# Kernel optimization log

Hardware: AMD Instinct MI355X
Metric: run time of the kernel (lower is better)

Reference implementation:

```python
import math
import jax, jax.numpy as jnp
import numpy as np

NUM_HEADS = 8
HEAD_DIM = 64


def setup_inputs() -> dict:
    key = jax.random.key(0)
    k1, k2, k3, k4 = jax.random.split(key, 4)
    C = 256
    E = NUM_HEADS * HEAD_DIM  # 512
    x = jax.random.normal(k1, (4, C, 48, 48), dtype=jnp.float32)
    Wqkv = jax.random.normal(k2, (3 * E, C), dtype=jnp.float32) * (1.0 / math.sqrt(C))
    Wout = jax.random.normal(k3, (C, E), dtype=jnp.float32) * (1.0 / math.sqrt(E))
    bout = jax.random.normal(k4, (C,), dtype=jnp.float32) * 0.01
    return {"x": x, "Wqkv": Wqkv, "Wout": Wout, "bout": bout}


def reference(x, Wqkv, Wout, bout):
    b, c, H, W = x.shape
    nh, hd = NUM_HEADS, HEAD_DIM
    N = H * W
    scale = 1.0 / math.sqrt(hd)
    # 1x1 conv (no bias) == channel matmul
    qkv = jnp.einsum('bcxy,oc->boxy', x, Wqkv)            # [b, 3*nh*hd, H, W]
    qkv = qkv.reshape(b, 3, nh, hd, N)                    # channel split order: (k, h, d)
    q, k, v = qkv[:, 0], qkv[:, 1], qkv[:, 2]             # each [b, nh, hd, N]
    att = jnp.einsum('bhdi,bhdj->bhij', q, k) * scale     # [b, nh, N, N]
    att = jax.nn.softmax(att, axis=-1)                    # stable (max-subtract inside)
    out = jnp.einsum('bhij,bhdj->bhid', att, v)           # [b, nh, N, hd]
    out = out.transpose(0, 1, 3, 2).reshape(b, nh * hd, H, W)  # 'b h (x y) d -> b (h d) x y'
    # 1x1 conv with bias
    return jnp.einsum('bexy,ce->bcxy', out, Wout) + bout[None, :, None, None]
```

## Files before the change

### kernel.cpp

```cpp
#include <hip/hip_runtime.h>

typedef __attribute__((ext_vector_type(8))) __bf16 bf16x8;
typedef __attribute__((ext_vector_type(16))) float f32x16;
typedef __attribute__((ext_vector_type(4))) float f32x4;
typedef __attribute__((ext_vector_type(4))) unsigned short us4;

__device__ __forceinline__ unsigned short f2bf(float f) {
  __bf16 h = (__bf16)f;
  return __builtin_bit_cast(unsigned short, h);
}
__device__ __forceinline__ unsigned pack2bf(float lo, float hi) {
  return (unsigned)f2bf(lo) | ((unsigned)f2bf(hi) << 16);
}

#define GLL(src, dst)                                                            \
  __builtin_amdgcn_global_load_lds((const __attribute__((address_space(1))) void*)(src), \
                                   (__attribute__((address_space(3))) void*)(dst), 16, 0, 0)

__device__ __forceinline__ void stage_chunks(const unsigned short* g, int ld,
                                             unsigned short* lds, int rows, int tid) {
  int total = rows * 8;
  for (int c0 = 0; c0 < total; c0 += 256) {
    int c = c0 + tid;
    int row = c >> 3, kc = c & 7;
    const unsigned short* src = g + (size_t)row * ld + ((kc ^ (row & 7)) << 3);
    unsigned short* dst = lds + (size_t)(c0 + (tid & 192)) * 8;
    GLL(src, dst);
  }
}

__device__ __forceinline__ bf16x8 frag(const unsigned short* lds, int row, int kc) {
  return *(const bf16x8*)(lds + row * 64 + ((kc ^ (row & 7)) << 3));
}


__global__ void k_cvt(const float* __restrict__ in, unsigned short* __restrict__ outp, int n) {
  int i = (blockIdx.x * 256 + threadIdx.x) * 4;
  if (i + 3 < n) {
    f32x4 v = *(const f32x4*)(in + i);
    us4 o;
#pragma unroll
    for (int k = 0; k < 4; k++) o[k] = f2bf(v[k]);
    *(us4*)(outp + i) = o;
  }
}

__global__ __launch_bounds__(256) void k_xpose(const float* __restrict__ x,
                                               unsigned short* __restrict__ xT) {
  __shared__ float t[32][33];
  int tid = threadIdx.x;
  int col = tid & 31, rowb = tid >> 5;
  int nt = blockIdx.x * 32, ct = blockIdx.y * 32, b = blockIdx.z;
  const float* src = x + ((size_t)b * 256 + ct) * 2304 + nt;
#pragma unroll
  for (int rr = 0; rr < 32; rr += 8) t[rowb + rr][col] = src[(size_t)(rowb + rr) * 2304 + col];
  __syncthreads();
  unsigned short* dst = xT + ((size_t)b * 2304 + nt) * 256 + ct;
#pragma unroll
  for (int rr = 0; rr < 32; rr += 8) dst[(size_t)(rowb + rr) * 256 + col] = f2bf(t[col][rowb + rr]);
}

__global__ __launch_bounds__(256, 2) void k_gemm_qkv(
    const unsigned short* __restrict__ W, const unsigned short* __restrict__ xT,
    unsigned short* __restrict__ qT, unsigned short* __restrict__ kT,
    unsigned short* __restrict__ vv) {
  __shared__ unsigned short As[128 * 64];
  __shared__ unsigned short Bs[128 * 64];
  int tid = threadIdx.x, lane = tid & 63, wid = tid >> 6;
  int m0 = blockIdx.x * 128, n0 = blockIdx.y * 128, b = blockIdx.z;
  const unsigned short* Ag = W + (size_t)m0 * 256;
  const unsigned short* Bg = xT + ((size_t)b * 2304 + n0) * 256;
  int wm = (wid >> 1) * 64, wn = (wid & 1) * 64;
  f32x4 acc[4][4] = {};
  for (int kt = 0; kt < 256; kt += 64) {
    __syncthreads();
    stage_chunks(Ag + kt, 256, As, 128, tid);
    stage_chunks(Bg + kt, 256, Bs, 128, tid);
    __syncthreads();
#pragma unroll
    for (int kk = 0; kk < 2; kk++) {
      bf16x8 af[4], bf[4];
#pragma unroll
      for (int i = 0; i < 4; i++) af[i] = frag(As, wm + i * 16 + (lane & 15), kk * 4 + (lane >> 4));
#pragma unroll
      for (int j = 0; j < 4; j++) bf[j] = frag(Bs, wn + j * 16 + (lane & 15), kk * 4 + (lane >> 4));
#pragma unroll
      for (int i = 0; i < 4; i++)
#pragma unroll
        for (int j = 0; j < 4; j++)
          acc[i][j] = __builtin_amdgcn_mfma_f32_16x16x32_bf16(af[i], bf[j], acc[i][j], 0, 0, 0);
    }
  }
#pragma unroll
  for (int i = 0; i < 4; i++) {
    int o = m0 + wm + i * 16 + ((lane >> 4) << 2);
    int which = o >> 9, h = (o >> 6) & 7, d0 = o & 63;
#pragma unroll
    for (int j = 0; j < 4; j++) {
      int n = n0 + wn + j * 16 + (lane & 15);
      if (which == 2) {
#pragma unroll
        for (int jj = 0; jj < 4; jj++)
          vv[((size_t)(b * 8 + h) * 64 + d0 + jj) * 2304 + n] = f2bf(acc[i][j][jj]);
      } else {
        float sc = which ? 1.0f : 0.18033688011112042f;
        us4 pk;
#pragma unroll
        for (int jj = 0; jj < 4; jj++) pk[jj] = f2bf(acc[i][j][jj] * sc);
        unsigned short* dst = (which ? kT : qT) + ((size_t)(b * 8 + h) * 2304 + n) * 64 + d0;
        *(us4*)dst = pk;
      }
    }
  }
}

__global__ __launch_bounds__(512, 4) void k_attn(
    const unsigned short* __restrict__ qT, const unsigned short* __restrict__ kT,
    const unsigned short* __restrict__ vv, unsigned short* __restrict__ o2T) {
  __shared__ unsigned short L[2][4][4096];
  int tid = threadIdx.x, lane = tid & 63;
  int wid = tid >> 6, rh = wid & 3, jh = wid >> 2;
  int il = lane & 31, g = lane >> 5;
  int lin = blockIdx.x;
  int xcd = lin & 7, idx = lin >> 3;
  int bh = xcd * 4 + idx / 18;
  int i0 = (idx % 18) * 128;
  const unsigned short* kT_bh = kT + (size_t)bh * 2304 * 64;
  const unsigned short* vv_bh = vv + (size_t)bh * 64 * 2304;
  const unsigned short* qrow = qT + ((size_t)bh * 2304 + i0 + rh * 32 + il) * 64;
  bf16x8 qf[4];
#pragma unroll
  for (int ks = 0; ks < 4; ks++) qf[ks] = *(const bf16x8*)(qrow + (ks * 2 + g) * 8);

  int srow = tid >> 3, skc = tid & 7;
  unsigned sw = (unsigned)((skc ^ (srow & 7)) << 3);
  unsigned oK = srow * 64 + sw;
  unsigned oV = srow * 2304 + sw;
  int db = (tid & 448) * 8;
  unsigned short* dK0 = &L[0][0][db];
  unsigned short* dK1 = &L[0][1][db];
  unsigned short* dV0 = &L[0][2][db];
  unsigned short* dV1 = &L[0][3][db];

#define STAGE(boff)                          \
  do {                                       \
    GLL(kT_bh + oK, dK0 + (boff));           \
    GLL(kT_bh + 73728 + oK, dK1 + (boff));   \
    GLL(vv_bh + oV, dV0 + (boff));           \
    GLL(vv_bh + 1152 + oV, dV1 + (boff));    \
    oK += 4096; oV += 64;                    \
  } while (0)

  const unsigned short* fK[8];
  const unsigned short* fV[8];
#pragma unroll
  for (int ks = 0; ks < 4; ks++) {
    int cs = ks * 2 + g;
    int o0 = il * 64 + ((cs ^ (il & 7)) << 3);
    int o1 = (32 + il) * 64 + ((cs ^ (il & 7)) << 3);
    fK[ks] = &L[0][jh][o0];
    fK[4 + ks] = &L[0][jh][o1];
    fV[ks] = &L[0][2 + jh][o0];
    fV[4 + ks] = &L[0][2 + jh][o1];
  }

  float lrun = 0.f;
  f32x16 O0 = {}, O1 = {};

#define COMP(boff)                                                                        \
  do {                                                                                    \
    f32x16 S0 = {}, S1 = {};                                                              \
    __builtin_amdgcn_s_setprio(1);                                                        \
    _Pragma("unroll") for (int ks = 0; ks < 4; ks++) {                                    \
      bf16x8 kf0 = *(const bf16x8*)(fK[ks] + (boff));                                     \
      bf16x8 kf1 = *(const bf16x8*)(fK[4 + ks] + (boff));                                 \
      S0 = __builtin_amdgcn_mfma_f32_32x32x16_bf16(kf0, qf[ks], S0, 0, 0, 0);             \
      S1 = __builtin_amdgcn_mfma_f32_32x32x16_bf16(kf1, qf[ks], S1, 0, 0, 0);             \
    }                                                                                     \
    __builtin_amdgcn_s_setprio(0);                                                        \
    float a16[16];                                                                        \
    _Pragma("unroll") for (int r = 0; r < 16; r++) {                                      \
      S0[r] = __builtin_amdgcn_exp2f(S0[r]);                                              \
      S1[r] = __builtin_amdgcn_exp2f(S1[r]);                                              \
      a16[r] = S0[r] + S1[r];                                                             \
    }                                                                                     \
    _Pragma("unroll") for (int s = 8; s >= 1; s >>= 1)                                    \
        _Pragma("unroll") for (int r = 0; r < 8; r++) if (r < s) a16[r] += a16[r + s];    \
    lrun += a16[0];                                                                       \
    unsigned w0[8], w1[8];                                                                \
    _Pragma("unroll") for (int m = 0; m < 8; m++) {                                       \
      w0[m] = pack2bf(S0[2 * m], S0[2 * m + 1]);                                          \
      w1[m] = pack2bf(S1[2 * m], S1[2 * m + 1]);                                          \
    }                                                                                     \
    __builtin_amdgcn_s_setprio(1);                                                        \
    _Pragma("unroll") for (int ks = 0; ks < 4; ks++) {                                    \
      int a = ks & 1;                                                                     \
      unsigned A0, A1, B0, B1;                                                            \
      if (ks >> 1) { A0 = w1[4 * a]; A1 = w1[4 * a + 1]; B0 = w1[4 * a + 2]; B1 = w1[4 * a + 3]; } \
      else         { A0 = w0[4 * a]; A1 = w0[4 * a + 1]; B0 = w0[4 * a + 2]; B1 = w0[4 * a + 3]; } \
      unsigned send0 = g ? A0 : B0, send1 = g ? A1 : B1;                                  \
      unsigned pw0 = __shfl_xor(send0, 32), pw1 = __shfl_xor(send1, 32);                  \
      union { unsigned u[4]; bf16x8 v; } F;                                               \
      F.u[0] = g ? pw0 : A0;                                                              \
      F.u[1] = g ? pw1 : A1;                                                              \
      F.u[2] = g ? B0 : pw0;                                                              \
      F.u[3] = g ? B1 : pw1;                                                              \
      bf16x8 vf0 = *(const bf16x8*)(fV[ks] + (boff));                                     \
      bf16x8 vf1 = *(const bf16x8*)(fV[4 + ks] + (boff));                                 \
      O0 = __builtin_amdgcn_mfma_f32_32x32x16_bf16(vf0, F.v, O0, 0, 0, 0);                \
      O1 = __builtin_amdgcn_mfma_f32_32x32x16_bf16(vf1, F.v, O1, 0, 0, 0);                \
    }                                                                                     \
    __builtin_amdgcn_s_setprio(0);                                                        \
  } while (0)

  STAGE(0);
  __syncthreads();
#pragma unroll 1
  for (int it = 0; it < 9; it++) {
    STAGE(16384);
    COMP(0);
    __syncthreads();
    if (it < 8) STAGE(0);
    COMP(16384);
    __syncthreads();
  }
#undef STAGE
#undef COMP

  lrun += __shfl_xor(lrun, 32);
  float* sm = (float*)&L[0][0][0];
  float* ml = (float*)&L[1][0][0];
  if (jh == 1) {
#pragma unroll
    for (int r = 0; r < 16; r++) {
      sm[(rh * 32 + r) * 64 + lane] = O0[r];
      sm[(rh * 32 + 16 + r) * 64 + lane] = O1[r];
    }
    if (!g) ml[rh * 32 + il] = lrun;
  }
  __syncthreads();
  if (jh == 0) {
    float rl = 1.0f / (lrun + ml[rh * 32 + il]);
    int b = bh >> 3, h = bh & 7;
    unsigned short* dst = o2T + ((size_t)b * 2304 + (i0 + rh * 32 + il)) * 512 + h * 64;
#pragma unroll
    for (int dt = 0; dt < 2; dt++) {
#pragma unroll
      for (int u = 0; u < 4; u++) {
        us4 pk;
#pragma unroll
        for (int v = 0; v < 4; v++) {
          int r = 4 * u + v;
          float own = dt ? O1[r] : O0[r];
          float oth = sm[(rh * 32 + dt * 16 + r) * 64 + lane];
          pk[v] = f2bf((own + oth) * rl);
        }
        *(us4*)(dst + dt * 32 + 8 * u + 4 * g) = pk;
      }
    }
  }
}

__global__ __launch_bounds__(256, 2) void k_gemm_out(
    const unsigned short* __restrict__ Wo, const unsigned short* __restrict__ o2T,
    const float* __restrict__ bout, float* __restrict__ out) {
  __shared__ unsigned short As[128 * 64];
  __shared__ unsigned short Bs[128 * 64];
  int tid = threadIdx.x, lane = tid & 63, wid = tid >> 6;
  int m0 = blockIdx.x * 128, n0 = blockIdx.y * 128, b = blockIdx.z;
  const unsigned short* Ag = Wo + (size_t)m0 * 512;
  const unsigned short* Bg = o2T + ((size_t)b * 2304 + n0) * 512;
  int wm = (wid >> 1) * 64, wn = (wid & 1) * 64;
  f32x4 acc[4][4] = {};
  for (int kt = 0; kt < 512; kt += 64) {
    __syncthreads();
    stage_chunks(Ag + kt, 512, As, 128, tid);
    stage_chunks(Bg + kt, 512, Bs, 128, tid);
    __syncthreads();
#pragma unroll
    for (int kk = 0; kk < 2; kk++) {
      bf16x8 af[4], bf[4];
#pragma unroll
      for (int i = 0; i < 4; i++) af[i] = frag(As, wm + i * 16 + (lane & 15), kk * 4 + (lane >> 4));
#pragma unroll
      for (int j = 0; j < 4; j++) bf[j] = frag(Bs, wn + j * 16 + (lane & 15), kk * 4 + (lane >> 4));
#pragma unroll
      for (int i = 0; i < 4; i++)
#pragma unroll
        for (int j = 0; j < 4; j++)
          acc[i][j] = __builtin_amdgcn_mfma_f32_16x16x32_bf16(af[i], bf[j], acc[i][j], 0, 0, 0);
    }
  }
#pragma unroll
  for (int i = 0; i < 4; i++) {
    int c = m0 + wm + i * 16 + ((lane >> 4) << 2);
#pragma unroll
    for (int j = 0; j < 4; j++) {
      int n = n0 + wn + j * 16 + (lane & 15);
#pragma unroll
      for (int jj = 0; jj < 4; jj++)
        out[((size_t)b * 256 + c + jj) * 2304 + n] = acc[i][j][jj] + bout[c + jj];
    }
  }
}

extern "C" void kernel_launch(void* const* d_in, const int* in_sizes, int n_in,
                              void* d_out, int out_size, void* d_ws, size_t ws_size,
                              hipStream_t stream) {
  const float* x = (const float*)d_in[0];
  const float* Wqkv = (const float*)d_in[1];
  const float* Wout = (const float*)d_in[2];
  const float* bout = (const float*)d_in[3];
  float* out = (float*)d_out;
  char* ws = (char*)d_ws;
  unsigned short* Wqkv_bf = (unsigned short*)(ws + 0);
  unsigned short* Wout_bf = (unsigned short*)(ws + 786432);
  unsigned short* xT      = (unsigned short*)(ws + 1048576);
  unsigned short* qT      = (unsigned short*)(ws + 5767168);
  unsigned short* kT      = (unsigned short*)(ws + 15204352);
  unsigned short* vv      = (unsigned short*)(ws + 24641536);
  unsigned short* o2T     = (unsigned short*)(ws + 34078720);

  k_cvt<<<dim3(384), dim3(256), 0, stream>>>(Wqkv, Wqkv_bf, 1536 * 256);
  k_cvt<<<dim3(128), dim3(256), 0, stream>>>(Wout, Wout_bf, 256 * 512);
  k_xpose<<<dim3(72, 8, 4), dim3(256), 0, stream>>>(x, xT);
  k_gemm_qkv<<<dim3(12, 18, 4), dim3(256), 0, stream>>>(Wqkv_bf, xT, qT, kT, vv);
  k_attn<<<dim3(576), dim3(512), 0, stream>>>(qT, kT, vv, o2T);
  k_gemm_out<<<dim3(2, 18, 4), dim3(256), 0, stream>>>(Wout_bf, o2T, bout, out);
}
```

Before: 111.5 us.

## Merge weight conversions, defer softmax row-sum reduction, halve out-GEMM N tile

Fuses the two fp32-to-bf16 weight conversion launches into one kernel, removing a launch. In attention, per-lane partial row sums are kept in 16 registers across all key tiles and tree-reduced once at the end instead of every iteration. The row-sum scratch moves to its own shared array, and a barrier is added before shared memory is reused. The output GEMM tile shrinks from 128 to 64 columns, doubling grid size to improve occupancy on the many-CU GPU at the cost of more reloads of A.

After: 118.8 us. 6.6% more time.

```diff
diff --git a/kernel.cpp b/kernel.cpp
--- a/kernel.cpp
+++ b/kernel.cpp
@@ -34,15 +34,20 @@
 }
 
 
-__global__ void k_cvt(const float* __restrict__ in, unsigned short* __restrict__ outp, int n) {
+__global__ void k_cvt2(const float* __restrict__ wqkv, const float* __restrict__ wout,
+                       unsigned short* __restrict__ oq, unsigned short* __restrict__ oo) {
+  const int NA = 1536 * 256;
   int i = (blockIdx.x * 256 + threadIdx.x) * 4;
-  if (i + 3 < n) {
-    f32x4 v = *(const f32x4*)(in + i);
-    us4 o;
-#pragma unroll
-    for (int k = 0; k < 4; k++) o[k] = f2bf(v[k]);
-    *(us4*)(outp + i) = o;
-  }
+  const float* src;
+  unsigned short* dst;
+  int j;
+  if (i < NA) { src = wqkv; dst = oq; j = i; }
+  else        { src = wout; dst = oo; j = i - NA; }
+  f32x4 v = *(const f32x4*)(src + j);
+  us4 o;
+#pragma unroll
+  for (int k = 0; k < 4; k++) o[k] = f2bf(v[k]);
+  *(us4*)(dst + j) = o;
 }
 
 __global__ __launch_bounds__(256) void k_xpose(const float* __restrict__ x,
@@ -118,6 +123,7 @@
     const unsigned short* __restrict__ qT, const unsigned short* __restrict__ kT,
     const unsigned short* __restrict__ vv, unsigned short* __restrict__ o2T) {
   __shared__ unsigned short L[2][4][4096];
+  __shared__ float ml[128];
   int tid = threadIdx.x, lane = tid & 63;
   int wid = tid >> 6, rh = wid & 3, jh = wid >> 2;
   int il = lane & 31, g = lane >> 5;
@@ -164,7 +170,7 @@
     fV[4 + ks] = &L[0][2 + jh][o1];
   }
 
-  float lrun = 0.f;
+  float a16[16] = {};
   f32x16 O0 = {}, O1 = {};
 
 #define COMP(boff)                                                                        \
@@ -178,15 +184,11 @@
       S1 = __builtin_amdgcn_mfma_f32_32x32x16_bf16(kf1, qf[ks], S1, 0, 0, 0);             \
     }                                                                                     \
     __builtin_amdgcn_s_setprio(0);                                                        \
-    float a16[16];                                                                        \
     _Pragma("unroll") for (int r = 0; r < 16; r++) {                                      \
       S0[r] = __builtin_amdgcn_exp2f(S0[r]);                                              \
       S1[r] = __builtin_amdgcn_exp2f(S1[r]);                                              \
-      a16[r] = S0[r] + S1[r];                                                             \
+      a16[r] += S0[r] + S1[r];                                                            \
     }                                                                                     \
-    _Pragma("unroll") for (int s = 8; s >= 1; s >>= 1)                                    \
-        _Pragma("unroll") for (int r = 0; r < 8; r++) if (r < s) a16[r] += a16[r + s];    \
-    lrun += a16[0];                                                                       \
     unsigned w0[8], w1[8];                                                                \
     _Pragma("unroll") for (int m = 0; m < 8; m++) {                                       \
       w0[m] = pack2bf(S0[2 * m], S0[2 * m + 1]);                                          \
@@ -227,9 +229,14 @@
 #undef STAGE
 #undef COMP
 
-  lrun += __shfl_xor(lrun, 32);
+#pragma unroll
+  for (int s = 8; s >= 1; s >>= 1)
+#pragma unroll
+    for (int r = 0; r < 8; r++)
+      if (r < s) a16[r] += a16[r + s];
+  float lrun = a16[0] + __shfl_xor(a16[0], 32);
+  __syncthreads();
   float* sm = (float*)&L[0][0][0];
-  float* ml = (float*)&L[1][0][0];
   if (jh == 1) {
 #pragma unroll
     for (int r = 0; r < 16; r++) {
@@ -265,29 +272,29 @@
     const unsigned short* __restrict__ Wo, const unsigned short* __restrict__ o2T,
     const float* __restrict__ bout, float* __restrict__ out) {
   __shared__ unsigned short As[128 * 64];
-  __shared__ unsigned short Bs[128 * 64];
+  __shared__ unsigned short Bs[64 * 64];
   int tid = threadIdx.x, lane = tid & 63, wid = tid >> 6;
-  int m0 = blockIdx.x * 128, n0 = blockIdx.y * 128, b = blockIdx.z;
+  int m0 = blockIdx.x * 128, n0 = blockIdx.y * 64, b = blockIdx.z;
   const unsigned short* Ag = Wo + (size_t)m0 * 512;
   const unsigned short* Bg = o2T + ((size_t)b * 2304 + n0) * 512;
-  int wm = (wid >> 1) * 64, wn = (wid & 1) * 64;
-  f32x4 acc[4][4] = {};
+  int wm = (wid >> 1) * 64, wn = (wid & 1) * 32;
+  f32x4 acc[4][2] = {};
   for (int kt = 0; kt < 512; kt += 64) {
     __syncthreads();
     stage_chunks(Ag + kt, 512, As, 128, tid);
-    stage_chunks(Bg + kt, 512, Bs, 128, tid);
+    stage_chunks(Bg + kt, 512, Bs, 64, tid);
     __syncthreads();
 #pragma unroll
     for (int kk = 0; kk < 2; kk++) {
-      bf16x8 af[4], bf[4];
+      bf16x8 af[4], bf[2];
 #pragma unroll
       for (int i = 0; i < 4; i++) af[i] = frag(As, wm + i * 16 + (lane & 15), kk * 4 + (lane >> 4));
 #pragma unroll
-      for (int j = 0; j < 4; j++) bf[j] = frag(Bs, wn + j * 16 + (lane & 15), kk * 4 + (lane >> 4));
+      for (int j = 0; j < 2; j++) bf[j] = frag(Bs, wn + j * 16 + (lane & 15), kk * 4 + (lane >> 4));
 #pragma unroll
       for (int i = 0; i < 4; i++)
 #pragma unroll
-        for (int j = 0; j < 4; j++)
+        for (int j = 0; j < 2; j++)
           acc[i][j] = __builtin_amdgcn_mfma_f32_16x16x32_bf16(af[i], bf[j], acc[i][j], 0, 0, 0);
     }
   }
@@ -295,7 +302,7 @@
   for (int i = 0; i < 4; i++) {
     int c = m0 + wm + i * 16 + ((lane >> 4) << 2);
 #pragma unroll
-    for (int j = 0; j < 4; j++) {
+    for (int j = 0; j < 2; j++) {
       int n = n0 + wn + j * 16 + (lane & 15);
 #pragma unroll
       for (int jj = 0; jj < 4; jj++)
@@ -321,10 +328,9 @@
   unsigned short* vv      = (unsigned short*)(ws + 24641536);
   unsigned short* o2T     = (unsigned short*)(ws + 34078720);
 
-  k_cvt<<<dim3(384), dim3(256), 0, stream>>>(Wqkv, Wqkv_bf, 1536 * 256);
-  k_cvt<<<dim3(128), dim3(256), 0, stream>>>(Wout, Wout_bf, 256 * 512);
+  k_cvt2<<<dim3(512), dim3(256), 0, stream>>>(Wqkv, Wout, Wqkv_bf, Wout_bf);
   k_xpose<<<dim3(72, 8, 4), dim3(256), 0, stream>>>(x, xT);
   k_gemm_qkv<<<dim3(12, 18, 4), dim3(256), 0, stream>>>(Wqkv_bf, xT, qT, kT, vv);
   k_attn<<<dim3(576), dim3(512), 0, stream>>>(qT, kT, vv, o2T);
-  k_gemm_out<<<dim3(2, 18, 4), dim3(256), 0, stream>>>(Wout_bf, o2T, bout, out);
-}
+  k_gemm_out<<<dim3(2, 36, 4), dim3(256), 0, stream>>>(Wout_bf, o2T, bout, out);
+}
```
